# Optimization experiments

Hardware: AMD Instinct MI355X
Metric: run time of the kernel (lower is better)

The kernel has to match this reference:

```python
import jax, jax.numpy as jnp
import numpy as np

B, F, N, S, D = 128, 3, 64, 96, 64  # batch, features, nodes, steps, d_model
DIN = F + 1  # delta_t channel appended inside forward


def _layer_norm(x, g, b, eps=1e-5):
    mu = jnp.mean(x, -1, keepdims=True)
    var = jnp.mean((x - mu) ** 2, -1, keepdims=True)
    return (x - mu) * jax.lax.rsqrt(var + eps) * g + b


def _encoder_layer(x, inw, inb, ow, ob, w1, b1, w2, b2, g1, be1, g2, be2):
    # x: (B, N, D). Torch post-norm TransformerEncoderLayer, nhead=1, eval mode (no dropout).
    q, k, v = jnp.split(x @ inw.T + inb, 3, axis=-1)
    scores = jnp.einsum('bnd,bmd->bnm', q, k) / jnp.sqrt(jnp.asarray(D, x.dtype))
    a = jnp.einsum('bnm,bmd->bnd', jax.nn.softmax(scores, -1), v) @ ow.T + ob
    x = _layer_norm(x + a, g1, be1)
    ff = jax.nn.relu(x @ w1.T + b1) @ w2.T + b2
    return _layer_norm(x + ff, g2, be2)


def _diff_conv(x, adj, w, b):
    x1 = jnp.einsum('bcv,wv->bcw', x, adj)
    x2 = jnp.einsum('bcv,wv->bcw', x1, adj)
    z = jnp.concatenate([x, x1, x2], axis=1)  # (B, 3C, N)
    return jnp.einsum('bcn,oc->bon', z, w) + b[None, :, None]


def _forward(x, adj, h0, tp, uw, ub, cw, cb):
    times = x[:, 2, 0, :]  # (B, S) timestamps
    dt = jnp.concatenate([jnp.zeros((B, 1), x.dtype), times[:, 1:] - times[:, :-1]], axis=1)  # (B, S)
    xs = (jnp.transpose(x, (3, 0, 1, 2)), jnp.transpose(dt)[:, :, None])  # (S,B,F,N), (S,B,1)

    def step(h, inp):
        xt, d = inp  # (B,F,N), (B,1)
        xin = jnp.concatenate([xt, jnp.broadcast_to(d[:, :, None], (B, 1, N))], axis=1)  # (B,DIN,N)
        y = jnp.transpose(h, (0, 2, 1))  # (B, N, D): nodes are the attention sequence
        for i in range(2):
            y = _encoder_layer(y, *(a[i] for a in tp))
        eps = jnp.transpose(y, (0, 2, 1))  # (B, D, N)
        hd = jnp.sqrt(1.0 - d)[:, :, None] * h - jnp.sqrt(d)[:, :, None] * eps
        xg = jnp.concatenate([xin, hd], axis=1)  # (B, DIN+D, N)
        u = jax.nn.sigmoid(_diff_conv(xg, adj, uw, ub))
        c = jnp.tanh(_diff_conv(xg, adj, cw, cb))
        hn = u * hd + (1.0 - u) * c
        return hn, hn

    _, outs = jax.lax.scan(step, h0, xs)  # (S, B, D, N)
    return jnp.transpose(outs, (1, 3, 2, 0))  # (B, N, D, S) == stack().permute(1,3,2,0)


def setup_inputs() -> dict:
    key = jax.random.key(0)
    ks = jax.random.split(key, 12)
    s = 0.05
    x = jax.random.normal(ks[0], (B, F, N, S), jnp.float32)
    inc = jax.random.uniform(ks[1], (B, S), jnp.float32, 0.001, 0.01)
    x = x.at[:, 2, 0, :].set(jnp.cumsum(inc, axis=1))  # monotone times, delta_t in (0, 0.01)
    adj = jax.random.uniform(ks[2], (N, N), jnp.float32)
    adj = adj / jnp.sum(adj, axis=1, keepdims=True)
    h0 = jax.random.normal(ks[3], (B, D, N), jnp.float32)
    lengths = jax.random.randint(ks[4], (B,), 1, S, jnp.int32)  # unused by forward
    return {
        'x': x, 'adj': adj, 'lengths': lengths, 'h0': h0,
        't_inw': jax.random.normal(ks[5], (2, 3 * D, D), jnp.float32) * s,
        't_inb': jnp.zeros((2, 3 * D), jnp.float32),
        't_ow': jax.random.normal(ks[6], (2, D, D), jnp.float32) * s,
        't_ob': jnp.zeros((2, D), jnp.float32),
        't_w1': jax.random.normal(ks[7], (2, 64, D), jnp.float32) * s,
        't_b1': jnp.zeros((2, 64), jnp.float32),
        't_w2': jax.random.normal(ks[8], (2, D, 64), jnp.float32) * s,
        't_b2': jnp.zeros((2, D), jnp.float32),
        't_g1': jnp.ones((2, D), jnp.float32), 't_be1': jnp.zeros((2, D), jnp.float32),
        't_g2': jnp.ones((2, D), jnp.float32), 't_be2': jnp.zeros((2, D), jnp.float32),
        'uw': jax.random.normal(ks[9], (D, 3 * (DIN + D)), jnp.float32) * s,
        'ub': jnp.zeros((D,), jnp.float32),
        'cw': jax.random.normal(ks[10], (D, 3 * (DIN + D)), jnp.float32) * s,
        'cb': jnp.zeros((D,), jnp.float32),
    }


def reference(x, adj, lengths, h0, t_inw, t_inb, t_ow, t_ob, t_w1, t_b1, t_w2, t_b2,
              t_g1, t_be1, t_g2, t_be2, uw, ub, cw, cb):
    tp = (t_inw, t_inb, t_ow, t_ob, t_w1, t_b1, t_w2, t_b2, t_g1, t_be1, t_g2, t_be2)
    return _forward(x, adj, h0, tp, uw, ub, cw, cb)
```

## Files before the change

kernel.cpp:

```cpp
#include <hip/hip_runtime.h>
#include <math.h>

#define TPB 512

typedef __attribute__((ext_vector_type(8))) short bf16x8;
typedef __attribute__((ext_vector_type(4))) float f32x4;
typedef unsigned short u16;

#define MFMA(a, b, c) __builtin_amdgcn_mfma_f32_16x16x32_bf16(a, b, c, 0, 0, 0)

__device__ __forceinline__ u16 f2bf(float f) {
  union { float f; unsigned u; } v; v.f = f;
  unsigned u = v.u;
  return (u16)((u + 0x7fffu + ((u >> 16) & 1u)) >> 16);
}
__device__ __forceinline__ float bf2f(u16 h) {
  union { unsigned u; float f; } v; v.u = ((unsigned)h) << 16; return v.f;
}
__device__ __forceinline__ unsigned cvt2(float a0, float a1) {
  return (unsigned)f2bf(a0) | ((unsigned)f2bf(a1) << 16);
}
__device__ __forceinline__ void cvt4u(float a0, float a1, float a2, float a3, u16 o[4]) {
  o[0] = f2bf(a0); o[1] = f2bf(a1); o[2] = f2bf(a2); o[3] = f2bf(a3);
}

__device__ __forceinline__ bf16x8 fragL(const u16* B, int row0, int pitch, int kb, int lane) {
  return *(const bf16x8*)(B + (row0 + (lane & 15)) * pitch + kb + ((lane >> 4) << 3));
}
__device__ __forceinline__ bf16x8 fragG(const float* __restrict__ W, int row0, int stride,
                                        int kb, int lane) {
  const float* p = W + (size_t)(row0 + (lane & 15)) * stride + kb + ((lane >> 4) << 3);
  float4 a = *(const float4*)p, b = *(const float4*)(p + 4);
  bf16x8 r;
  r[0] = (short)f2bf(a.x); r[1] = (short)f2bf(a.y); r[2] = (short)f2bf(a.z); r[3] = (short)f2bf(a.w);
  r[4] = (short)f2bf(b.x); r[5] = (short)f2bf(b.y); r[6] = (short)f2bf(b.z); r[7] = (short)f2bf(b.w);
  return r;
}
template<int PREW>
__device__ __forceinline__ bf16x8 wfrag(const float* __restrict__ Wg,
                                        const u16* __restrict__ Wp,
                                        int m, int f, int kh, int lane) {
  if constexpr (PREW)
    return *(const bf16x8*)(Wp + (size_t)m * 4096 + f * 1024 + kh * 512 + lane * 8);
  else
    return fragG(Wg, f * 16, 64, kh * 32, lane);
}

__global__ __launch_bounds__(256)
void prep_kernel(const float* __restrict__ t_inw, const float* __restrict__ t_ow,
                 const float* __restrict__ t_w1, const float* __restrict__ t_w2,
                 const float* __restrict__ adj, const float* __restrict__ x,
                 u16* __restrict__ wp, u16* __restrict__ wpA2,
                 float* __restrict__ wsDT, u16* __restrict__ wsX) {
  int m = blockIdx.x;
  if (m == 12) {
    __shared__ float a2[4096];
    for (int e = threadIdx.x; e < 4096; e += 256) {
      int w = e >> 6, u = e & 63;
      float sum = 0.f;
      for (int v = 0; v < 64; ++v) sum += adj[w * 64 + v] * adj[v * 64 + u];
      a2[e] = sum;
    }
    __syncthreads();
    for (int t = threadIdx.x; t < 4096; t += 256) {
      int j = t & 7, ln = (t >> 3) & 63, kh = (t >> 9) & 1, f = t >> 10;
      int row = f * 16 + (ln & 15);
      int k = kh * 32 + ((ln >> 4) << 3) + j;
      wpA2[t] = f2bf(a2[row * 64 + k]);
    }
    return;
  }
  if (m >= 13) {
    int b = m - 13;
    const float* times = x + ((size_t)b * 3 + 2) * 64 * 96;
    for (int i = threadIdx.x; i < 96 * 256; i += 256) {
      int s = i >> 8, idx = i & 255, f = idx >> 6, n = idx & 63;
      float v;
      if (f < 3) v = x[(((size_t)b * 3 + f) * 64 + n) * 96 + s];
      else {
        float dt = s ? (times[s] - times[s - 1]) : 0.f;
        v = dt;
        if (n == 0) wsDT[b * 96 + s] = dt;
      }
      wsX[((size_t)b * 96 + s) * 256 + idx] = f2bf(v);
    }
    return;
  }
  int l = m / 6, r = m % 6;
  const float* W;
  if (r < 3)       W = t_inw + l * 12288 + r * 4096;
  else if (r == 3) W = t_ow + l * 4096;
  else if (r == 4) W = t_w1 + l * 4096;
  else             W = t_w2 + l * 4096;
  for (int t = threadIdx.x; t < 4096; t += 256) {
    int j = t & 7, ln = (t >> 3) & 63, kh = (t >> 9) & 1, f = t >> 10;
    int row = f * 16 + (ln & 15);
    int k = kh * 32 + ((ln >> 4) << 3) + j;
    wp[(size_t)m * 4096 + t] = f2bf(W[row * 64 + k]);
  }
}

__global__ __launch_bounds__(TPB, 2)
void gcrnn_fast(const float* __restrict__ adj,
                const float* __restrict__ h0,
                const float* __restrict__ t_inb, const float* __restrict__ t_ob,
                const float* __restrict__ t_b1,  const float* __restrict__ t_b2,
                const float* __restrict__ t_g1,  const float* __restrict__ t_be1,
                const float* __restrict__ t_g2,  const float* __restrict__ t_be2,
                const float* __restrict__ uw,    const float* __restrict__ ub,
                const float* __restrict__ cw,    const float* __restrict__ cb,
                const u16* __restrict__ wsW,  const u16* __restrict__ wsA2,
                const float* __restrict__ wsDT, const u16* __restrict__ wsX,
                float* __restrict__ wsOut)
{
  const int b = blockIdx.x;
  const int tid = threadIdx.x;
  const int wv = tid >> 6;
  const int lane = tid & 63;
  const int lx = lane & 15;
  const int gq = (lane >> 4) << 2;
  const int rs = wv & 3;
  const int of0 = (wv >> 2) * 2;
  const int fA = wv >> 2;

  __shared__ __align__(16) u16 adjB[64 * 72];
  __shared__ __align__(16) u16 Y0[64 * 72];
  __shared__ __align__(16) u16 Y1[64 * 72];
  __shared__ __align__(16) u16 Qb[64 * 72];
  __shared__ __align__(16) u16 Kb[64 * 72];
  __shared__ __align__(16) u16 VTb[64 * 72];
  __shared__ __align__(16) u16 Pb[64 * 72];
  __shared__ __align__(16) u16 xgB[80 * 72];
  __shared__ __align__(16) u16 zTB[64 * 232];
  __shared__ __align__(16) u16 uwcwB[2 * 4 * 7 * 512];

  float hreg[2][4];
  {
    const int nb = rs * 16 + gq;
#pragma unroll
    for (int ff = 0; ff < 2; ++ff) {
      int o = (of0 + ff) * 16 + lx;
      float4 hv = *(const float4*)(h0 + (size_t)b * 4096 + o * 64 + nb);
#pragma unroll
      for (int j = 0; j < 4; ++j) {
        hreg[ff][j] = (&hv.x)[j];
        Y0[(nb + j) * 72 + o] = f2bf(hreg[ff][j]);
      }
    }
  }
  for (int i = tid; i < 4096; i += TPB)
    adjB[(i >> 6) * 72 + (i & 63)] = f2bf(adj[i]);
  for (int i = tid; i < 2 * 4 * 7 * 512; i += TPB) {
    int t = i;
    int j = t & 7; t >>= 3;
    int ln = t & 63; t >>= 6;
    int kh = t % 7; t /= 7;
    int f = t & 3; int mat = t >> 2;
    int o = f * 16 + (ln & 15);
    int k = kh * 32 + ((ln >> 4) << 3) + j;
    const float* W = mat ? cw : uw;
    uwcwB[i] = (k < 204) ? f2bf(W[o * 204 + k]) : (u16)0;
  }
  for (int i = tid; i < 64 * 28; i += TPB)
    zTB[(i / 28) * 232 + 204 + (i % 28)] = 0;
  for (int i = tid; i < 12 * 72; i += TPB)
    xgB[68 * 72 + i] = 0;
  __syncthreads();

  const float buo = ub[of0 * 16 + lx], buo2 = ub[(of0 + 1) * 16 + lx];
  const float bco = cb[of0 * 16 + lx], bco2 = cb[(of0 + 1) * 16 + lx];
  float hdreg[2][4];

  for (int s = 0; s < 96; ++s) {
    float dcur = wsDT[b * 96 + s];
    float sq1 = sqrtf(1.f - dcur), sq2 = sqrtf(dcur);

    for (int l = 0; l < 2; ++l) {
      const int l6 = l * 6;
      const float* inb = t_inb + l * 192;
      const float* ob  = t_ob  + l * 64;
      const float* bb1 = t_b1  + l * 64;
      const float* bb2 = t_b2  + l * 64;
      const float* g1  = t_g1  + l * 64;
      const float* be1 = t_be1 + l * 64;
      const float* g2  = t_g2  + l * 64;
      const float* be2 = t_be2 + l * 64;

      bf16x8 fq[2][2], fk[2][2], fw1r[2][2], fvr[2];
#pragma unroll
      for (int fi = 0; fi < 2; ++fi)
#pragma unroll
        for (int kh = 0; kh < 2; ++kh) {
          fq[fi][kh]   = wfrag<1>(nullptr, wsW, l6 + 0, fA + fi * 2, kh, lane);
          fk[fi][kh]   = wfrag<1>(nullptr, wsW, l6 + 1, fA + fi * 2, kh, lane);
          fw1r[fi][kh] = wfrag<1>(nullptr, wsW, l6 + 4, fA + fi * 2, kh, lane);
        }
      if (wv >= 4) {
#pragma unroll
        for (int kh = 0; kh < 2; ++kh)
          fvr[kh] = wfrag<1>(nullptr, wsW, l6 + 2, rs, kh, lane);
      }

      {
        bf16x8 a0 = fragL(Y0, rs * 16, 72, 0, lane);
        bf16x8 a1 = fragL(Y0, rs * 16, 72, 32, lane);
#pragma unroll
        for (int fi = 0; fi < 2; ++fi) {
          int f = fA + fi * 2;
          int col = f * 16 + lx;
          {
            f32x4 acc = {0.f, 0.f, 0.f, 0.f};
            acc = MFMA(a0, fq[fi][0], acc);
            acc = MFMA(a1, fq[fi][1], acc);
            float bv = inb[col];
            u16 o4[4]; cvt4u(acc[0] + bv, acc[1] + bv, acc[2] + bv, acc[3] + bv, o4);
#pragma unroll
            for (int j = 0; j < 4; ++j)
              Qb[(rs * 16 + gq + j) * 72 + col] = o4[j];
          }
          {
            f32x4 acc = {0.f, 0.f, 0.f, 0.f};
            acc = MFMA(a0, fk[fi][0], acc);
            acc = MFMA(a1, fk[fi][1], acc);
            float bv = inb[64 + col];
            u16 o4[4]; cvt4u(acc[0] + bv, acc[1] + bv, acc[2] + bv, acc[3] + bv, o4);
#pragma unroll
            for (int j = 0; j < 4; ++j)
              Kb[(rs * 16 + gq + j) * 72 + col] = o4[j];
          }
        }
      }
      __syncthreads();

      if (wv < 4) {
        bf16x8 qa0 = fragL(Qb, rs * 16, 72, 0, lane);
        bf16x8 qa1 = fragL(Qb, rs * 16, 72, 32, lane);
        f32x4 sc[4];
#pragma unroll
        for (int f = 0; f < 4; ++f) {
          f32x4 acc = {0.f, 0.f, 0.f, 0.f};
          acc = MFMA(qa0, fragL(Kb, f * 16, 72, 0, lane), acc);
          acc = MFMA(qa1, fragL(Kb, f * 16, 72, 32, lane), acc);
#pragma unroll
          for (int j = 0; j < 4; ++j) acc[j] *= 0.125f;
          sc[f] = acc;
        }
#pragma unroll
        for (int j = 0; j < 4; ++j) {
          float m1 = fmaxf(fmaxf(sc[0][j], sc[1][j]), fmaxf(sc[2][j], sc[3][j]));
          m1 = fmaxf(m1, __shfl_xor(m1, 1));
          m1 = fmaxf(m1, __shfl_xor(m1, 2));
          m1 = fmaxf(m1, __shfl_xor(m1, 4));
          m1 = fmaxf(m1, __shfl_xor(m1, 8));
          float s1 = 0.f;
#pragma unroll
          for (int f = 0; f < 4; ++f) { float e = __expf(sc[f][j] - m1); sc[f][j] = e; s1 += e; }
          s1 += __shfl_xor(s1, 1); s1 += __shfl_xor(s1, 2);
          s1 += __shfl_xor(s1, 4); s1 += __shfl_xor(s1, 8);
          float inv = 1.f / s1;
          int row = rs * 16 + gq + j;
          u16 o4[4];
          cvt4u(sc[0][j] * inv, sc[1][j] * inv, sc[2][j] * inv, sc[3][j] * inv, o4);
#pragma unroll
          for (int f = 0; f < 4; ++f)
            Pb[row * 72 + f * 16 + lx] = o4[f];
        }
      } else {
#pragma unroll
        for (int f = 0; f < 4; ++f) {
          f32x4 acc = {0.f, 0.f, 0.f, 0.f};
          acc = MFMA(fvr[0], fragL(Y0, f * 16, 72, 0, lane), acc);
          acc = MFMA(fvr[1], fragL(Y0, f * 16, 72, 32, lane), acc);
          int dd0 = rs * 16 + gq;
          u16 o4[4];
          cvt4u(acc[0] + inb[128 + dd0], acc[1] + inb[128 + dd0 + 1],
                acc[2] + inb[128 + dd0 + 2], acc[3] + inb[128 + dd0 + 3], o4);
#pragma unroll
          for (int j = 0; j < 4; ++j)
            VTb[(dd0 + j) * 72 + f * 16 + lx] = o4[j];
        }
      }
      __syncthreads();

      bf16x8 fo[4][2];
      if (wv < 4) {
#pragma unroll
        for (int f = 0; f < 4; ++f)
#pragma unroll
          for (int kh = 0; kh < 2; ++kh)
            fo[f][kh] = wfrag<1>(nullptr, wsW, l6 + 3, f, kh, lane);
      }
      {
        bf16x8 pa0 = fragL(Pb, rs * 16, 72, 0, lane);
        bf16x8 pa1 = fragL(Pb, rs * 16, 72, 32, lane);
#pragma unroll
        for (int fi = 0; fi < 2; ++fi) {
          int f = fA + fi * 2;
          f32x4 acc = {0.f, 0.f, 0.f, 0.f};
          acc = MFMA(pa0, fragL(VTb, f * 16, 72, 0, lane), acc);
          acc = MFMA(pa1, fragL(VTb, f * 16, 72, 32, lane), acc);
          u16 o4[4]; cvt4u(acc[0], acc[1], acc[2], acc[3], o4);
#pragma unroll
          for (int j = 0; j < 4; ++j)
            Qb[(rs * 16 + gq + j) * 72 + f * 16 + lx] = o4[j];
        }
      }
      __syncthreads();

      if (wv < 4) {
        bf16x8 a0 = fragL(Qb, rs * 16, 72, 0, lane);
        bf16x8 a1 = fragL(Qb, rs * 16, 72, 32, lane);
        float t4[4][4];
#pragma unroll
        for (int f = 0; f < 4; ++f) {
          f32x4 acc = {0.f, 0.f, 0.f, 0.f};
          acc = MFMA(a0, fo[f][0], acc);
          acc = MFMA(a1, fo[f][1], acc);
          int col = f * 16 + lx;
          float bv = ob[col];
#pragma unroll
          for (int j = 0; j < 4; ++j) {
            int row = rs * 16 + gq + j;
            t4[f][j] = acc[j] + bv + bf2f(Y0[row * 72 + col]);
          }
        }
#pragma unroll
        for (int j = 0; j < 4; ++j) {
          float s1 = t4[0][j] + t4[1][j] + t4[2][j] + t4[3][j];
          float s2 = t4[0][j] * t4[0][j] + t4[1][j] * t4[1][j]
                   + t4[2][j] * t4[2][j] + t4[3][j] * t4[3][j];
          s1 += __shfl_xor(s1, 1); s2 += __shfl_xor(s2, 1);
          s1 += __shfl_xor(s1, 2); s2 += __shfl_xor(s2, 2);
          s1 += __shfl_xor(s1, 4); s2 += __shfl_xor(s2, 4);
          s1 += __shfl_xor(s1, 8); s2 += __shfl_xor(s2, 8);
          float mu = s1 * 0.015625f;
          float rstd = rsqrtf(s2 * 0.015625f - mu * mu + 1e-5f);
          int row = rs * 16 + gq + j;
          u16 o4[4];
          cvt4u((t4[0][j] - mu) * rstd * g1[0 * 16 + lx] + be1[0 * 16 + lx],
                (t4[1][j] - mu) * rstd * g1[1 * 16 + lx] + be1[1 * 16 + lx],
                (t4[2][j] - mu) * rstd * g1[2 * 16 + lx] + be1[2 * 16 + lx],
                (t4[3][j] - mu) * rstd * g1[3 * 16 + lx] + be1[3 * 16 + lx], o4);
#pragma unroll
          for (int f = 0; f < 4; ++f)
            Y1[row * 72 + f * 16 + lx] = o4[f];
        }
      }
      __syncthreads();

      bf16x8 fw2[4][2];
#pragma unroll
      for (int f = 0; f < 4; ++f)
#pragma unroll
        for (int kh = 0; kh < 2; ++kh)
          fw2[f][kh] = wfrag<1>(nullptr, wsW, l6 + 5, f, kh, lane);
      {
        bf16x8 a0 = fragL(Y1, rs * 16, 72, 0, lane);
        bf16x8 a1 = fragL(Y1, rs * 16, 72, 32, lane);
#pragma unroll
        for (int fi = 0; fi < 2; ++fi) {
          int f = fA + fi * 2;
          f32x4 acc = {0.f, 0.f, 0.f, 0.f};
          acc = MFMA(a0, fw1r[fi][0], acc);
          acc = MFMA(a1, fw1r[fi][1], acc);
          int col = f * 16 + lx;
          float bv = bb1[col];
          u16 o4[4];
          cvt4u(fmaxf(acc[0] + bv, 0.f), fmaxf(acc[1] + bv, 0.f),
                fmaxf(acc[2] + bv, 0.f), fmaxf(acc[3] + bv, 0.f), o4);
#pragma unroll
          for (int j = 0; j < 4; ++j)
            Kb[(rs * 16 + gq + j) * 72 + col] = o4[j];
        }
      }
      __syncthreads();

      if (l == 0) {
        if (wv < 4) {
          bf16x8 a0 = fragL(Kb, rs * 16, 72, 0, lane);
          bf16x8 a1 = fragL(Kb, rs * 16, 72, 32, lane);
          float t4[4][4];
#pragma unroll
          for (int f = 0; f < 4; ++f) {
            f32x4 acc = {0.f, 0.f, 0.f, 0.f};
            acc = MFMA(a0, fw2[f][0], acc);
            acc = MFMA(a1, fw2[f][1], acc);
            int col = f * 16 + lx;
            float bv = bb2[col];
#pragma unroll
            for (int j = 0; j < 4; ++j) {
              int row = rs * 16 + gq + j;
              t4[f][j] = acc[j] + bv + bf2f(Y1[row * 72 + col]);
            }
          }
#pragma unroll
          for (int j = 0; j < 4; ++j) {
            float s1 = t4[0][j] + t4[1][j] + t4[2][j] + t4[3][j];
            float s2 = t4[0][j] * t4[0][j] + t4[1][j] * t4[1][j]
                     + t4[2][j] * t4[2][j] + t4[3][j] * t4[3][j];
            s1 += __shfl_xor(s1, 1); s2 += __shfl_xor(s2, 1);
            s1 += __shfl_xor(s1, 2); s2 += __shfl_xor(s2, 2);
            s1 += __shfl_xor(s1, 4); s2 += __shfl_xor(s2, 4);
            s1 += __shfl_xor(s1, 8); s2 += __shfl_xor(s2, 8);
            float mu = s1 * 0.015625f;
            float rstd = rsqrtf(s2 * 0.015625f - mu * mu + 1e-5f);
            int row = rs * 16 + gq + j;
            u16 o4[4];
            cvt4u((t4[0][j] - mu) * rstd * g2[0 * 16 + lx] + be2[0 * 16 + lx],
                  (t4[1][j] - mu) * rstd * g2[1 * 16 + lx] + be2[1 * 16 + lx],
                  (t4[2][j] - mu) * rstd * g2[2 * 16 + lx] + be2[2 * 16 + lx],
                  (t4[3][j] - mu) * rstd * g2[3 * 16 + lx] + be2[3 * 16 + lx], o4);
#pragma unroll
            for (int f = 0; f < 4; ++f)
              Y0[row * 72 + f * 16 + lx] = o4[f];
          }
        }
      } else {
        bf16x8 a0 = fragL(Kb, rs * 16, 72, 0, lane);
        bf16x8 a1 = fragL(Kb, rs * 16, 72, 32, lane);
        float t4[4][4];
#pragma unroll
        for (int f = 0; f < 4; ++f) {
          f32x4 acc = {0.f, 0.f, 0.f, 0.f};
          acc = MFMA(a0, fw2[f][0], acc);
          acc = MFMA(a1, fw2[f][1], acc);
          int col = f * 16 + lx;
          float bv = bb2[col];
#pragma unroll
          for (int j = 0; j < 4; ++j) {
            int row = rs * 16 + gq + j;
            t4[f][j] = acc[j] + bv + bf2f(Y1[row * 72 + col]);
          }
        }
#pragma unroll
        for (int j = 0; j < 4; ++j) {
          float s1 = t4[0][j] + t4[1][j] + t4[2][j] + t4[3][j];
          float s2 = t4[0][j] * t4[0][j] + t4[1][j] * t4[1][j]
                   + t4[2][j] * t4[2][j] + t4[3][j] * t4[3][j];
          s1 += __shfl_xor(s1, 1); s2 += __shfl_xor(s2, 1);
          s1 += __shfl_xor(s1, 2); s2 += __shfl_xor(s2, 2);
          s1 += __shfl_xor(s1, 4); s2 += __shfl_xor(s2, 4);
          s1 += __shfl_xor(s1, 8); s2 += __shfl_xor(s2, 8);
          float mu = s1 * 0.015625f;
          float rstd = rsqrtf(s2 * 0.015625f - mu * mu + 1e-5f);
#pragma unroll
          for (int f = 0; f < 4; ++f) {
            int col = f * 16 + lx;
            t4[f][j] = (t4[f][j] - mu) * rstd * g2[col] + be2[col];
          }
        }
        {
          const u16* xr = wsX + ((size_t)b * 96 + s) * 256;
          for (int i = tid; i < 256; i += TPB) {
            u16 v = xr[i];
            int f = i >> 6, n = i & 63;
            xgB[f * 72 + n] = v;
            zTB[n * 232 + f] = v;
          }
        }
        const int nb = rs * 16 + gq;
#pragma unroll
        for (int f = 0; f < 4; ++f) {
          if ((f >> 1) == (wv >> 2)) {
            const int ff = f & 1;
            int o = f * 16 + lx;
            float hd0 = sq1 * hreg[ff][0] - sq2 * t4[f][0];
            float hd1 = sq1 * hreg[ff][1] - sq2 * t4[f][1];
            float hd2 = sq1 * hreg[ff][2] - sq2 * t4[f][2];
            float hd3 = sq1 * hreg[ff][3] - sq2 * t4[f][3];
            hdreg[ff][0] = hd0; hdreg[ff][1] = hd1;
            hdreg[ff][2] = hd2; hdreg[ff][3] = hd3;
            unsigned p0 = cvt2(hd0, hd1), p1 = cvt2(hd2, hd3);
            zTB[(nb + 0) * 232 + 4 + o] = (u16)p0;
            zTB[(nb + 1) * 232 + 4 + o] = (u16)(p0 >> 16);
            zTB[(nb + 2) * 232 + 4 + o] = (u16)p1;
            zTB[(nb + 3) * 232 + 4 + o] = (u16)(p1 >> 16);
            uint2 pk; pk.x = p0; pk.y = p1;
            *(uint2*)(xgB + (4 + o) * 72 + nb) = pk;
          }
        }
      }
      __syncthreads();
    }

    f32x4 aU0 = {0.f,0.f,0.f,0.f}, aU1 = {0.f,0.f,0.f,0.f};
    f32x4 aC0 = {0.f,0.f,0.f,0.f}, aC1 = {0.f,0.f,0.f,0.f};
    {
      bf16x8 g0 = *(const bf16x8*)(wsA2 + rs * 1024 + lane * 8);
      bf16x8 g1 = *(const bf16x8*)(wsA2 + rs * 1024 + 512 + lane * 8);
      bf16x8 aj0 = fragL(adjB, rs * 16, 72, 0, lane);
      bf16x8 aj1 = fragL(adjB, rs * 16, 72, 32, lane);

#define HT(A0, A1, CF, OFF) { \
      f32x4 acc = {0.f,0.f,0.f,0.f}; \
      acc = MFMA(A0, fragL(xgB, (CF) * 16, 72, 0, lane), acc); \
      acc = MFMA(A1, fragL(xgB, (CF) * 16, 72, 32, lane), acc); \
      int c = (CF) * 16 + lx; \
      if (c < 68) { u16 o4[4]; cvt4u(acc[0], acc[1], acc[2], acc[3], o4); \
        _Pragma("unroll") for (int j = 0; j < 4; ++j) \
          zTB[(rs * 16 + gq + j) * 232 + (OFF) + c] = o4[j]; } }

#define J01 { _Pragma("unroll") for (int kh = 0; kh < 2; ++kh) { \
      bf16x8 a = fragL(zTB, rs * 16, 232, kh * 32, lane); \
      { const u16* pu = uwcwB + (size_t)((of0 + 0) * 7 + kh) * 512 + lane * 8; \
        const u16* pc = uwcwB + (size_t)((4 + of0 + 0) * 7 + kh) * 512 + lane * 8; \
        aU0 = MFMA(a, *(const bf16x8*)pu, aU0); \
        aC0 = MFMA(a, *(const bf16x8*)pc, aC0); } \
      { const u16* pu = uwcwB + (size_t)((of0 + 1) * 7 + kh) * 512 + lane * 8; \
        const u16* pc = uwcwB + (size_t)((4 + of0 + 1) * 7 + kh) * 512 + lane * 8; \
        aU1 = MFMA(a, *(const bf16x8*)pu, aU1); \
        aC1 = MFMA(a, *(const bf16x8*)pc, aC1); } } }

      if (wv < 4) {
        HT(aj0, aj1, 0, 68); HT(aj0, aj1, 2, 68); HT(aj0, aj1, 4, 68);
        J01;
        HT(g0, g1, 1, 136); HT(g0, g1, 3, 136);
      } else {
        HT(aj0, aj1, 1, 68); HT(aj0, aj1, 3, 68);
        J01;
        HT(g0, g1, 0, 136); HT(g0, g1, 2, 136); HT(g0, g1, 4, 136);
      }
#undef HT
#undef J01
    }
    __syncthreads();

    {
#pragma unroll
      for (int kh = 2; kh < 7; ++kh) {
        bf16x8 a = fragL(zTB, rs * 16, 232, kh * 32, lane);
        {
          const u16* pu = uwcwB + (size_t)((of0 + 0) * 7 + kh) * 512 + lane * 8;
          const u16* pc = uwcwB + (size_t)((4 + of0 + 0) * 7 + kh) * 512 + lane * 8;
          aU0 = MFMA(a, *(const bf16x8*)pu, aU0);
          aC0 = MFMA(a, *(const bf16x8*)pc, aC0);
        }
        {
          const u16* pu = uwcwB + (size_t)((of0 + 1) * 7 + kh) * 512 + lane * 8;
          const u16* pc = uwcwB + (size_t)((4 + of0 + 1) * 7 + kh) * 512 + lane * 8;
          aU1 = MFMA(a, *(const bf16x8*)pu, aU1);
          aC1 = MFMA(a, *(const bf16x8*)pc, aC1);
        }
      }
      const int nb = rs * 16 + gq;
#pragma unroll
      for (int ff = 0; ff < 2; ++ff) {
        f32x4 aU = ff ? aU1 : aU0;
        f32x4 aC = ff ? aC1 : aC0;
        float bu_ = ff ? buo2 : buo;
        float bc_ = ff ? bco2 : bco;
        int o = (of0 + ff) * 16 + lx;
        float4 ov;
#pragma unroll
        for (int j = 0; j < 4; ++j) {
          float u = 1.f / (1.f + __expf(-(aU[j] + bu_)));
          float z = aC[j] + bc_;
          z = fminf(fmaxf(z, -15.f), 15.f);
          float e2 = __expf(2.f * z);
          float cval = (e2 - 1.f) / (e2 + 1.f);
          float hn = u * hdreg[ff][j] + (1.f - u) * cval;
          hreg[ff][j] = hn;
          (&ov.x)[j] = hn;
        }
        unsigned pk0 = cvt2(ov.x, ov.y), pk1 = cvt2(ov.z, ov.w);
        Y0[(nb + 0) * 72 + o] = (u16)pk0;
        Y0[(nb + 1) * 72 + o] = (u16)(pk0 >> 16);
        Y0[(nb + 2) * 72 + o] = (u16)pk1;
        Y0[(nb + 3) * 72 + o] = (u16)(pk1 >> 16);
        *(float4*)(wsOut + ((size_t)b * 96 + s) * 4096 + o * 64 + nb) = ov;
      }
    }
    __syncthreads();
  }
}

__global__ __launch_bounds__(TPB, 2)
void gcrnn_fb(const float* __restrict__ x, const float* __restrict__ adj,
              const float* __restrict__ h0,
              const float* __restrict__ t_inw, const float* __restrict__ t_inb,
              const float* __restrict__ t_ow,  const float* __restrict__ t_ob,
              const float* __restrict__ t_w1,  const float* __restrict__ t_b1,
              const float* __restrict__ t_w2,  const float* __restrict__ t_b2,
              const float* __restrict__ t_g1,  const float* __restrict__ t_be1,
              const float* __restrict__ t_g2,  const float* __restrict__ t_be2,
              const float* __restrict__ uw,    const float* __restrict__ ub,
              const float* __restrict__ cw,    const float* __restrict__ cb,
              float* __restrict__ out)
{
  const int b = blockIdx.x;
  const int tid = threadIdx.x;
  const int wv = tid >> 6;
  const int lane = tid & 63;
  const int lx = lane & 15;
  const int gq = (lane >> 4) << 2;
  const int rs = wv & 3;
  const int of0 = (wv >> 2) * 2;
  const int fA = wv >> 2;

  __shared__ __align__(16) u16 adjB[64 * 72];
  __shared__ __align__(16) u16 adj2B[64 * 72];
  __shared__ __align__(16) u16 ysB[64 * 72];
  __shared__ __align__(16) u16 pool[4 * 4608];
  __shared__ __align__(16) u16 zTB[64 * 232];
  __shared__ __align__(16) u16 uwcwB[2 * 4 * 7 * 512];

  u16* Qb  = pool;
  u16* Kb  = pool + 4608;
  u16* VTb = pool + 9216;
  u16* Pb  = pool + 13824;
  u16* xgB = pool;

  float hreg[2][4];
  {
    const int nb = rs * 16 + gq;
#pragma unroll
    for (int ff = 0; ff < 2; ++ff) {
      int o = (of0 + ff) * 16 + lx;
      float4 hv = *(const float4*)(h0 + (size_t)b * 4096 + o * 64 + nb);
#pragma unroll
      for (int j = 0; j < 4; ++j) {
        hreg[ff][j] = (&hv.x)[j];
        ysB[(nb + j) * 72 + o] = f2bf(hreg[ff][j]);
      }
    }
  }
  for (int i = tid; i < 4096; i += TPB)
    adjB[(i >> 6) * 72 + (i & 63)] = f2bf(adj[i]);
  for (int i = tid; i < 4096; i += TPB) {
    int w = i >> 6, u = i & 63;
    float sum = 0.f;
    for (int v = 0; v < 64; ++v) sum += adj[w * 64 + v] * adj[v * 64 + u];
    adj2B[w * 72 + u] = f2bf(sum);
  }
  for (int i = tid; i < 2 * 4 * 7 * 512; i += TPB) {
    int t = i;
    int j = t & 7; t >>= 3;
    int ln = t & 63; t >>= 6;
    int kh = t % 7; t /= 7;
    int f = t & 3; int mat = t >> 2;
    int o = f * 16 + (ln & 15);
    int k = kh * 32 + ((ln >> 4) << 3) + j;
    const float* W = mat ? cw : uw;
    uwcwB[i] = (k < 204) ? f2bf(W[o * 204 + k]) : (u16)0;
  }
  for (int i = tid; i < 64 * 28; i += TPB)
    zTB[(i / 28) * 232 + 204 + (i % 28)] = 0;
  __syncthreads();

  const float* times = x + ((size_t)b * 3 + 2) * 64 * 96;
  float hdreg[2][4];

  for (int s = 0; s < 96; ++s) {
    float dcur = (s == 0) ? 0.f : (times[s] - times[s - 1]);
    float sq1 = sqrtf(1.f - dcur), sq2 = sqrtf(dcur);

    for (int l = 0; l < 2; ++l) {
      const float* inw = t_inw + l * 12288;
      const float* inb = t_inb + l * 192;
      const float* ow  = t_ow  + l * 4096;
      const float* ob  = t_ob  + l * 64;
      const float* w1  = t_w1  + l * 4096;
      const float* bb1 = t_b1  + l * 64;
      const float* w2  = t_w2  + l * 4096;
      const float* bb2 = t_b2  + l * 64;
      const float* g1  = t_g1  + l * 64;
      const float* be1 = t_be1 + l * 64;
      const float* g2  = t_g2  + l * 64;
      const float* be2 = t_be2 + l * 64;

      {
        bf16x8 a0 = fragL(ysB, rs * 16, 72, 0, lane);
        bf16x8 a1 = fragL(ysB, rs * 16, 72, 32, lane);
#pragma unroll
        for (int fi = 0; fi < 2; ++fi) {
          int f = fA + fi * 2;
          int col = f * 16 + lx;
          {
            f32x4 acc = {0.f, 0.f, 0.f, 0.f};
            acc = MFMA(a0, fragG(inw, f * 16, 64, 0, lane), acc);
            acc = MFMA(a1, fragG(inw, f * 16, 64, 32, lane), acc);
            float bv = inb[col];
            u16 o4[4]; cvt4u(acc[0] + bv, acc[1] + bv, acc[2] + bv, acc[3] + bv, o4);
#pragma unroll
            for (int j = 0; j < 4; ++j)
              Qb[(rs * 16 + gq + j) * 72 + col] = o4[j];
          }
          {
            f32x4 acc = {0.f, 0.f, 0.f, 0.f};
            acc = MFMA(a0, fragG(inw + 4096, f * 16, 64, 0, lane), acc);
            acc = MFMA(a1, fragG(inw + 4096, f * 16, 64, 32, lane), acc);
            float bv = inb[64 + col];
            u16 o4[4]; cvt4u(acc[0] + bv, acc[1] + bv, acc[2] + bv, acc[3] + bv, o4);
#pragma unroll
            for (int j = 0; j < 4; ++j)
              Kb[(rs * 16 + gq + j) * 72 + col] = o4[j];
          }
        }
      }
      __syncthreads();

      if (wv < 4) {
        bf16x8 qa0 = fragL(Qb, rs * 16, 72, 0, lane);
        bf16x8 qa1 = fragL(Qb, rs * 16, 72, 32, lane);
        f32x4 sc[4];
#pragma unroll
        for (int f = 0; f < 4; ++f) {
          f32x4 acc = {0.f, 0.f, 0.f, 0.f};
          acc = MFMA(qa0, fragL(Kb, f * 16, 72, 0, lane), acc);
          acc = MFMA(qa1, fragL(Kb, f * 16, 72, 32, lane), acc);
#pragma unroll
          for (int j = 0; j < 4; ++j) acc[j] *= 0.125f;
          sc[f] = acc;
        }
#pragma unroll
        for (int j = 0; j < 4; ++j) {
          float m1 = fmaxf(fmaxf(sc[0][j], sc[1][j]), fmaxf(sc[2][j], sc[3][j]));
          m1 = fmaxf(m1, __shfl_xor(m1, 1));
          m1 = fmaxf(m1, __shfl_xor(m1, 2));
          m1 = fmaxf(m1, __shfl_xor(m1, 4));
          m1 = fmaxf(m1, __shfl_xor(m1, 8));
          float s1 = 0.f;
#pragma unroll
          for (int f = 0; f < 4; ++f) { float e = __expf(sc[f][j] - m1); sc[f][j] = e; s1 += e; }
          s1 += __shfl_xor(s1, 1); s1 += __shfl_xor(s1, 2);
          s1 += __shfl_xor(s1, 4); s1 += __shfl_xor(s1, 8);
          float inv = 1.f / s1;
          int row = rs * 16 + gq + j;
          u16 o4[4];
          cvt4u(sc[0][j] * inv, sc[1][j] * inv, sc[2][j] * inv, sc[3][j] * inv, o4);
#pragma unroll
          for (int f = 0; f < 4; ++f)
            Pb[row * 72 + f * 16 + lx] = o4[f];
        }
      } else {
        bf16x8 wa0 = fragG(inw + 8192, rs * 16, 64, 0, lane);
        bf16x8 wa1 = fragG(inw + 8192, rs * 16, 64, 32, lane);
#pragma unroll
        for (int f = 0; f < 4; ++f) {
          f32x4 acc = {0.f, 0.f, 0.f, 0.f};
          acc = MFMA(wa0, fragL(ysB, f * 16, 72, 0, lane), acc);
          acc = MFMA(wa1, fragL(ysB, f * 16, 72, 32, lane), acc);
          int dd0 = rs * 16 + gq;
          u16 o4[4];
          cvt4u(acc[0] + inb[128 + dd0], acc[1] + inb[128 + dd0 + 1],
                acc[2] + inb[128 + dd0 + 2], acc[3] + inb[128 + dd0 + 3], o4);
#pragma unroll
          for (int j = 0; j < 4; ++j)
            VTb[(dd0 + j) * 72 + f * 16 + lx] = o4[j];
        }
      }
      __syncthreads();

      {
        bf16x8 pa0 = fragL(Pb, rs * 16, 72, 0, lane);
        bf16x8 pa1 = fragL(Pb, rs * 16, 72, 32, lane);
#pragma unroll
        for (int fi = 0; fi < 2; ++fi) {
          int f = fA + fi * 2;
          f32x4 acc = {0.f, 0.f, 0.f, 0.f};
          acc = MFMA(pa0, fragL(VTb, f * 16, 72, 0, lane), acc);
          acc = MFMA(pa1, fragL(VTb, f * 16, 72, 32, lane), acc);
          u16 o4[4]; cvt4u(acc[0], acc[1], acc[2], acc[3], o4);
#pragma unroll
          for (int j = 0; j < 4; ++j)
            Qb[(rs * 16 + gq + j) * 72 + f * 16 + lx] = o4[j];
        }
      }
      __syncthreads();

      if (wv < 4) {
        bf16x8 a0 = fragL(Qb, rs * 16, 72, 0, lane);
        bf16x8 a1 = fragL(Qb, rs * 16, 72, 32, lane);
        float t4[4][4];
#pragma unroll
        for (int f = 0; f < 4; ++f) {
          f32x4 acc = {0.f, 0.f, 0.f, 0.f};
          acc = MFMA(a0, fragG(ow, f * 16, 64, 0, lane), acc);
          acc = MFMA(a1, fragG(ow, f * 16, 64, 32, lane), acc);
          int col = f * 16 + lx;
          float bv = ob[col];
#pragma unroll
          for (int j = 0; j < 4; ++j) {
            int row = rs * 16 + gq + j;
            t4[f][j] = acc[j] + bv + bf2f(ysB[row * 72 + col]);
          }
        }
#pragma unroll
        for (int j = 0; j < 4; ++j) {
          float s1 = t4[0][j] + t4[1][j] + t4[2][j] + t4[3][j];
          float s2 = t4[0][j] * t4[0][j] + t4[1][j] * t4[1][j]
                   + t4[2][j] * t4[2][j] + t4[3][j] * t4[3][j];
          s1 += __shfl_xor(s1, 1); s2 += __shfl_xor(s2, 1);
          s1 += __shfl_xor(s1, 2); s2 += __shfl_xor(s2, 2);
          s1 += __shfl_xor(s1, 4); s2 += __shfl_xor(s2, 4);
          s1 += __shfl_xor(s1, 8); s2 += __shfl_xor(s2, 8);
          float mu = s1 * 0.015625f;
          float rstd = rsqrtf(s2 * 0.015625f - mu * mu + 1e-5f);
          int row = rs * 16 + gq + j;
          u16 o4[4];
          cvt4u((t4[0][j] - mu) * rstd * g1[0 * 16 + lx] + be1[0 * 16 + lx],
                (t4[1][j] - mu) * rstd * g1[1 * 16 + lx] + be1[1 * 16 + lx],
                (t4[2][j] - mu) * rstd * g1[2 * 16 + lx] + be1[2 * 16 + lx],
                (t4[3][j] - mu) * rstd * g1[3 * 16 + lx] + be1[3 * 16 + lx], o4);
#pragma unroll
          for (int f = 0; f < 4; ++f)
            ysB[row * 72 + f * 16 + lx] = o4[f];
        }
      }
      __syncthreads();

      {
        bf16x8 a0 = fragL(ysB, rs * 16, 72, 0, lane);
        bf16x8 a1 = fragL(ysB, rs * 16, 72, 32, lane);
#pragma unroll
        for (int fi = 0; fi < 2; ++fi) {
          int f = fA + fi * 2;
          f32x4 acc = {0.f, 0.f, 0.f, 0.f};
          acc = MFMA(a0, fragG(w1, f * 16, 64, 0, lane), acc);
          acc = MFMA(a1, fragG(w1, f * 16, 64, 32, lane), acc);
          int col = f * 16 + lx;
          float bv = bb1[col];
          u16 o4[4];
          cvt4u(fmaxf(acc[0] + bv, 0.f), fmaxf(acc[1] + bv, 0.f),
                fmaxf(acc[2] + bv, 0.f), fmaxf(acc[3] + bv, 0.f), o4);
#pragma unroll
          for (int j = 0; j < 4; ++j)
            Kb[(rs * 16 + gq + j) * 72 + col] = o4[j];
        }
      }
      __syncthreads();

      if (wv < 4) {
        bf16x8 a0 = fragL(Kb, rs * 16, 72, 0, lane);
        bf16x8 a1 = fragL(Kb, rs * 16, 72, 32, lane);
        float t4[4][4];
#pragma unroll
        for (int f = 0; f < 4; ++f) {
          f32x4 acc = {0.f, 0.f, 0.f, 0.f};
          acc = MFMA(a0, fragG(w2, f * 16, 64, 0, lane), acc);
          acc = MFMA(a1, fragG(w2, f * 16, 64, 32, lane), acc);
          int col = f * 16 + lx;
          float bv = bb2[col];
#pragma unroll
          for (int j = 0; j < 4; ++j) {
            int row = rs * 16 + gq + j;
            t4[f][j] = acc[j] + bv + bf2f(ysB[row * 72 + col]);
          }
        }
#pragma unroll
        for (int j = 0; j < 4; ++j) {
          float s1 = t4[0][j] + t4[1][j] + t4[2][j] + t4[3][j];
          float s2 = t4[0][j] * t4[0][j] + t4[1][j] * t4[1][j]
                   + t4[2][j] * t4[2][j] + t4[3][j] * t4[3][j];
          s1 += __shfl_xor(s1, 1); s2 += __shfl_xor(s2, 1);
          s1 += __shfl_xor(s1, 2); s2 += __shfl_xor(s2, 2);
          s1 += __shfl_xor(s1, 4); s2 += __shfl_xor(s2, 4);
          s1 += __shfl_xor(s1, 8); s2 += __shfl_xor(s2, 8);
          float mu = s1 * 0.015625f;
          float rstd = rsqrtf(s2 * 0.015625f - mu * mu + 1e-5f);
          int row = rs * 16 + gq + j;
          u16 o4[4];
          cvt4u((t4[0][j] - mu) * rstd * g2[0 * 16 + lx] + be2[0 * 16 + lx],
                (t4[1][j] - mu) * rstd * g2[1 * 16 + lx] + be2[1 * 16 + lx],
                (t4[2][j] - mu) * rstd * g2[2 * 16 + lx] + be2[2 * 16 + lx],
                (t4[3][j] - mu) * rstd * g2[3 * 16 + lx] + be2[3 * 16 + lx], o4);
#pragma unroll
          for (int f = 0; f < 4; ++f)
            ysB[row * 72 + f * 16 + lx] = o4[f];
        }
      }
      __syncthreads();
    }

    {
      for (int i = tid; i < 256; i += TPB) {
        int f = i >> 6, n = i & 63;
        float v = (f < 3) ? x[(((size_t)b * 3 + f) * 64 + n) * 96 + s] : dcur;
        u16 v16 = f2bf(v);
        xgB[f * 72 + n] = v16;
        zTB[n * 232 + f] = v16;
      }
      const int nb = rs * 16 + gq;
#pragma unroll
      for (int ff = 0; ff < 2; ++ff) {
        int o = (of0 + ff) * 16 + lx;
        float hd0 = sq1 * hreg[ff][0] - sq2 * bf2f(ysB[(nb + 0) * 72 + o]);
        float hd1 = sq1 * hreg[ff][1] - sq2 * bf2f(ysB[(nb + 1) * 72 + o]);
        float hd2 = sq1 * hreg[ff][2] - sq2 * bf2f(ysB[(nb + 2) * 72 + o]);
        float hd3 = sq1 * hreg[ff][3] - sq2 * bf2f(ysB[(nb + 3) * 72 + o]);
        hdreg[ff][0] = hd0; hdreg[ff][1] = hd1; hdreg[ff][2] = hd2; hdreg[ff][3] = hd3;
        unsigned p0 = cvt2(hd0, hd1), p1 = cvt2(hd2, hd3);
        zTB[(nb + 0) * 232 + 4 + o] = (u16)p0;
        zTB[(nb + 1) * 232 + 4 + o] = (u16)(p0 >> 16);
        zTB[(nb + 2) * 232 + 4 + o] = (u16)p1;
        zTB[(nb + 3) * 232 + 4 + o] = (u16)(p1 >> 16);
        uint2 pk; pk.x = p0; pk.y = p1;
        *(uint2*)(xgB + (4 + o) * 72 + nb) = pk;
      }
    }
    __syncthreads();

    for (int t = wv; t < 40; t += 8) {
      int which = (t >= 20) ? 1 : 0;
      int tt = t - which * 20;
      int rw = tt & 3, cf = tt >> 2;
      const u16* A = which ? adj2B : adjB;
      f32x4 acc = {0.f, 0.f, 0.f, 0.f};
      acc = MFMA(fragL(A, rw * 16, 72, 0, lane), fragL(xgB, cf * 16, 72, 0, lane), acc);
      acc = MFMA(fragL(A, rw * 16, 72, 32, lane), fragL(xgB, cf * 16, 72, 32, lane), acc);
      int c = cf * 16 + lx;
      if (c < 68) {
        u16 o4[4]; cvt4u(acc[0], acc[1], acc[2], acc[3], o4);
#pragma unroll
        for (int j = 0; j < 4; ++j)
          zTB[(rw * 16 + gq + j) * 232 + 68 + which * 68 + c] = o4[j];
      }
    }
    __syncthreads();

    {
      f32x4 aU[2] = {{0.f,0.f,0.f,0.f},{0.f,0.f,0.f,0.f}};
      f32x4 aC[2] = {{0.f,0.f,0.f,0.f},{0.f,0.f,0.f,0.f}};
#pragma unroll
      for (int kh = 0; kh < 7; ++kh) {
        bf16x8 a = fragL(zTB, rs * 16, 232, kh * 32, lane);
#pragma unroll
        for (int ff = 0; ff < 2; ++ff) {
          int f = of0 + ff;
          const u16* pu = uwcwB + (size_t)((0 * 4 + f) * 7 + kh) * 512 + lane * 8;
          const u16* pc = uwcwB + (size_t)((1 * 4 + f) * 7 + kh) * 512 + lane * 8;
          aU[ff] = MFMA(a, *(const bf16x8*)pu, aU[ff]);
          aC[ff] = MFMA(a, *(const bf16x8*)pc, aC[ff]);
        }
      }
      const int nb = rs * 16 + gq;
#pragma unroll
      for (int ff = 0; ff < 2; ++ff) {
        int o = (of0 + ff) * 16 + lx;
        float bu_ = ub[o], bc_ = cb[o];
        float4 ov;
#pragma unroll
        for (int j = 0; j < 4; ++j) {
          float u = 1.f / (1.f + __expf(-(aU[ff][j] + bu_)));
          float z = aC[ff][j] + bc_;
          z = fminf(fmaxf(z, -15.f), 15.f);
          float e2 = __expf(2.f * z);
          float cval = (e2 - 1.f) / (e2 + 1.f);
          float hn = u * hdreg[ff][j] + (1.f - u) * cval;
          hreg[ff][j] = hn;
          (&ov.x)[j] = hn;
        }
        unsigned pk0 = cvt2(ov.x, ov.y), pk1 = cvt2(ov.z, ov.w);
        ysB[(nb + 0) * 72 + o] = (u16)pk0;
        ysB[(nb + 1) * 72 + o] = (u16)(pk0 >> 16);
        ysB[(nb + 2) * 72 + o] = (u16)pk1;
        ysB[(nb + 3) * 72 + o] = (u16)(pk1 >> 16);
#pragma unroll
        for (int j = 0; j < 4; ++j)
          out[((size_t)(b * 64 + (nb + j)) * 64 + o) * 96 + s] = (&ov.x)[j];
      }
    }
    __syncthreads();
  }
}

__global__ __launch_bounds__(256)
void transp_kernel(const float* __restrict__ ws, float* __restrict__ out) {
  int blk = blockIdx.x;
  int b = blk >> 6, o = blk & 63;
  __shared__ float t[96 * 68];
  for (int i = threadIdx.x; i < 96 * 64; i += 256) {
    int ss = i >> 6, n = i & 63;
    t[ss * 68 + n] = ws[((size_t)b * 96 + ss) * 4096 + o * 64 + n];
  }
  __syncthreads();
  for (int i = threadIdx.x; i < 64 * 96; i += 256) {
    int n = i / 96, ss = i - n * 96;
    out[((size_t)(b * 64 + n) * 64 + o) * 96 + ss] = t[ss * 68 + n];
  }
}

extern "C" void kernel_launch(void* const* d_in, const int* in_sizes, int n_in,
                              void* d_out, int out_size, void* d_ws, size_t ws_size,
                              hipStream_t stream)
{
  (void)in_sizes; (void)n_in; (void)out_size;
  const float* x     = (const float*)d_in[0];
  const float* adj   = (const float*)d_in[1];
  const float* h0    = (const float*)d_in[3];
  const float* t_inw = (const float*)d_in[4];
  const float* t_inb = (const float*)d_in[5];
  const float* t_ow  = (const float*)d_in[6];
  const float* t_ob  = (const float*)d_in[7];
  const float* t_w1  = (const float*)d_in[8];
  const float* t_b1  = (const float*)d_in[9];
  const float* t_w2  = (const float*)d_in[10];
  const float* t_b2  = (const float*)d_in[11];
  const float* t_g1  = (const float*)d_in[12];
  const float* t_be1 = (const float*)d_in[13];
  const float* t_g2  = (const float*)d_in[14];
  const float* t_be2 = (const float*)d_in[15];
  const float* uw    = (const float*)d_in[16];
  const float* ub    = (const float*)d_in[17];
  const float* cw    = (const float*)d_in[18];
  const float* cb    = (const float*)d_in[19];
  float* out = (float*)d_out;

  const size_t offA2    = 98304;
  const size_t offDT    = 106496;
  const size_t offX     = 155648;
  const size_t offStage = 6447104;
  const size_t stageBytes = (size_t)128 * 96 * 4096 * 4;

  if (ws_size >= offStage + stageBytes) {
    u16*   wsW   = (u16*)d_ws;
    u16*   wsA2  = (u16*)((char*)d_ws + offA2);
    float* wsDT  = (float*)((char*)d_ws + offDT);
    u16*   wsX   = (u16*)((char*)d_ws + offX);
    float* wsOut = (float*)((char*)d_ws + offStage);

    hipLaunchKernelGGL(prep_kernel, dim3(141), dim3(256), 0, stream,
                       t_inw, t_ow, t_w1, t_w2, adj, x, wsW, wsA2, wsDT, wsX);
    hipLaunchKernelGGL(gcrnn_fast, dim3(128), dim3(TPB), 0, stream,
                       adj, h0, t_inb, t_ob, t_b1, t_b2, t_g1, t_be1, t_g2, t_be2,
                       uw, ub, cw, cb, wsW, wsA2, wsDT, wsX, wsOut);
    hipLaunchKernelGGL(transp_kernel, dim3(128 * 64), dim3(256), 0, stream, wsOut, out);
  } else {
    hipLaunchKernelGGL(gcrnn_fb, dim3(128), dim3(TPB), 0, stream,
                       x, adj, h0, t_inw, t_inb, t_ow, t_ob, t_w1, t_b1,
                       t_w2, t_b2, t_g1, t_be1, t_g2, t_be2, uw, ub, cw, cb, out);
  }
}
```

Baseline: 1.498 ms.

## Give each wave full row-strips to drop intra-layer and diffusion-conv barriers

```diff
diff --git a/kernel.cpp b/kernel.cpp
--- a/kernel.cpp
+++ b/kernel.cpp
@@ -186,14 +186,13 @@
       const float* g2  = t_g2  + l * 64;
       const float* be2 = t_be2 + l * 64;
 
-      bf16x8 fq[2][2], fk[2][2], fw1r[2][2], fvr[2];
+      bf16x8 fq[2][2], fk[2][2], fvr[2];
 #pragma unroll
       for (int fi = 0; fi < 2; ++fi)
 #pragma unroll
         for (int kh = 0; kh < 2; ++kh) {
-          fq[fi][kh]   = wfrag<1>(nullptr, wsW, l6 + 0, fA + fi * 2, kh, lane);
-          fk[fi][kh]   = wfrag<1>(nullptr, wsW, l6 + 1, fA + fi * 2, kh, lane);
-          fw1r[fi][kh] = wfrag<1>(nullptr, wsW, l6 + 4, fA + fi * 2, kh, lane);
+          fq[fi][kh] = wfrag<1>(nullptr, wsW, l6 + 0, fA + fi * 2, kh, lane);
+          fk[fi][kh] = wfrag<1>(nullptr, wsW, l6 + 1, fA + fi * 2, kh, lane);
         }
       if (wv >= 4) {
 #pragma unroll
@@ -282,101 +281,93 @@
       }
       __syncthreads();
 
-      bf16x8 fo[4][2];
       if (wv < 4) {
+        bf16x8 fo[4][2], fw1[4][2];
 #pragma unroll
         for (int f = 0; f < 4; ++f)
 #pragma unroll
-          for (int kh = 0; kh < 2; ++kh)
-            fo[f][kh] = wfrag<1>(nullptr, wsW, l6 + 3, f, kh, lane);
-      }
-      {
-        bf16x8 pa0 = fragL(Pb, rs * 16, 72, 0, lane);
-        bf16x8 pa1 = fragL(Pb, rs * 16, 72, 32, lane);
-#pragma unroll
-        for (int fi = 0; fi < 2; ++fi) {
-          int f = fA + fi * 2;
-          f32x4 acc = {0.f, 0.f, 0.f, 0.f};
-          acc = MFMA(pa0, fragL(VTb, f * 16, 72, 0, lane), acc);
-          acc = MFMA(pa1, fragL(VTb, f * 16, 72, 32, lane), acc);
-          u16 o4[4]; cvt4u(acc[0], acc[1], acc[2], acc[3], o4);
-#pragma unroll
-          for (int j = 0; j < 4; ++j)
-            Qb[(rs * 16 + gq + j) * 72 + f * 16 + lx] = o4[j];
-        }
-      }
-      __syncthreads();
-
-      if (wv < 4) {
-        bf16x8 a0 = fragL(Qb, rs * 16, 72, 0, lane);
-        bf16x8 a1 = fragL(Qb, rs * 16, 72, 32, lane);
-        float t4[4][4];
-#pragma unroll
-        for (int f = 0; f < 4; ++f) {
-          f32x4 acc = {0.f, 0.f, 0.f, 0.f};
-          acc = MFMA(a0, fo[f][0], acc);
-          acc = MFMA(a1, fo[f][1], acc);
-          int col = f * 16 + lx;
-          float bv = ob[col];
+          for (int kh = 0; kh < 2; ++kh) {
+            fo[f][kh]  = wfrag<1>(nullptr, wsW, l6 + 3, f, kh, lane);
+            fw1[f][kh] = wfrag<1>(nullptr, wsW, l6 + 4, f, kh, lane);
+          }
+        {
+          bf16x8 pa0 = fragL(Pb, rs * 16, 72, 0, lane);
+          bf16x8 pa1 = fragL(Pb, rs * 16, 72, 32, lane);
+#pragma unroll
+          for (int f = 0; f < 4; ++f) {
+            f32x4 acc = {0.f, 0.f, 0.f, 0.f};
+            acc = MFMA(pa0, fragL(VTb, f * 16, 72, 0, lane), acc);
+            acc = MFMA(pa1, fragL(VTb, f * 16, 72, 32, lane), acc);
+            u16 o4[4]; cvt4u(acc[0], acc[1], acc[2], acc[3], o4);
+#pragma unroll
+            for (int j = 0; j < 4; ++j)
+              Qb[(rs * 16 + gq + j) * 72 + f * 16 + lx] = o4[j];
+          }
+        }
+        {
+          bf16x8 a0 = fragL(Qb, rs * 16, 72, 0, lane);
+          bf16x8 a1 = fragL(Qb, rs * 16, 72, 32, lane);
+          float t4[4][4];
+#pragma unroll
+          for (int f = 0; f < 4; ++f) {
+            f32x4 acc = {0.f, 0.f, 0.f, 0.f};
+            acc = MFMA(a0, fo[f][0], acc);
+            acc = MFMA(a1, fo[f][1], acc);
+            int col = f * 16 + lx;
+            float bv = ob[col];
+#pragma unroll
+            for (int j = 0; j < 4; ++j) {
+              int row = rs * 16 + gq + j;
+              t4[f][j] = acc[j] + bv + bf2f(Y0[row * 72 + col]);
+            }
+          }
 #pragma unroll
           for (int j = 0; j < 4; ++j) {
+            float s1 = t4[0][j] + t4[1][j] + t4[2][j] + t4[3][j];
+            float s2 = t4[0][j] * t4[0][j] + t4[1][j] * t4[1][j]
+                     + t4[2][j] * t4[2][j] + t4[3][j] * t4[3][j];
+            s1 += __shfl_xor(s1, 1); s2 += __shfl_xor(s2, 1);
+            s1 += __shfl_xor(s1, 2); s2 += __shfl_xor(s2, 2);
+            s1 += __shfl_xor(s1, 4); s2 += __shfl_xor(s2, 4);
+            s1 += __shfl_xor(s1, 8); s2 += __shfl_xor(s2, 8);
+            float mu = s1 * 0.015625f;
+            float rstd = rsqrtf(s2 * 0.015625f - mu * mu + 1e-5f);
             int row = rs * 16 + gq + j;
-            t4[f][j] = acc[j] + bv + bf2f(Y0[row * 72 + col]);
-          }
-        }
-#pragma unroll
-        for (int j = 0; j < 4; ++j) {
-          float s1 = t4[0][j] + t4[1][j] + t4[2][j] + t4[3][j];
-          float s2 = t4[0][j] * t4[0][j] + t4[1][j] * t4[1][j]
-                   + t4[2][j] * t4[2][j] + t4[3][j] * t4[3][j];
-          s1 += __shfl_xor(s1, 1); s2 += __shfl_xor(s2, 1);
-          s1 += __shfl_xor(s1, 2); s2 += __shfl_xor(s2, 2);
-          s1 += __shfl_xor(s1, 4); s2 += __shfl_xor(s2, 4);
-          s1 += __shfl_xor(s1, 8); s2 += __shfl_xor(s2, 8);
-          float mu = s1 * 0.015625f;
-          float rstd = rsqrtf(s2 * 0.015625f - mu * mu + 1e-5f);
-          int row = rs * 16 + gq + j;
-          u16 o4[4];
-          cvt4u((t4[0][j] - mu) * rstd * g1[0 * 16 + lx] + be1[0 * 16 + lx],
-                (t4[1][j] - mu) * rstd * g1[1 * 16 + lx] + be1[1 * 16 + lx],
-                (t4[2][j] - mu) * rstd * g1[2 * 16 + lx] + be1[2 * 16 + lx],
-                (t4[3][j] - mu) * rstd * g1[3 * 16 + lx] + be1[3 * 16 + lx], o4);
+            u16 o4[4];
+            cvt4u((t4[0][j] - mu) * rstd * g1[0 * 16 + lx] + be1[0 * 16 + lx],
+                  (t4[1][j] - mu) * rstd * g1[1 * 16 + lx] + be1[1 * 16 + lx],
+                  (t4[2][j] - mu) * rstd * g1[2 * 16 + lx] + be1[2 * 16 + lx],
+                  (t4[3][j] - mu) * rstd * g1[3 * 16 + lx] + be1[3 * 16 + lx], o4);
+#pragma unroll
+            for (int f = 0; f < 4; ++f)
+              Y1[row * 72 + f * 16 + lx] = o4[f];
+          }
+        }
+        {
+          bf16x8 a0 = fragL(Y1, rs * 16, 72, 0, lane);
+          bf16x8 a1 = fragL(Y1, rs * 16, 72, 32, lane);
+#pragma unroll
+          for (int f = 0; f < 4; ++f) {
+            f32x4 acc = {0.f, 0.f, 0.f, 0.f};
+            acc = MFMA(a0, fw1[f][0], acc);
+            acc = MFMA(a1, fw1[f][1], acc);
+            int col = f * 16 + lx;
+            float bv = bb1[col];
+            u16 o4[4];
+            cvt4u(fmaxf(acc[0] + bv, 0.f), fmaxf(acc[1] + bv, 0.f),
+                  fmaxf(acc[2] + bv, 0.f), fmaxf(acc[3] + bv, 0.f), o4);
+#pragma unroll
+            for (int j = 0; j < 4; ++j)
+              Kb[(rs * 16 + gq + j) * 72 + col] = o4[j];
+          }
+        }
+        if (l == 0) {
+          bf16x8 fw2[4][2];
 #pragma unroll
           for (int f = 0; f < 4; ++f)
-            Y1[row * 72 + f * 16 + lx] = o4[f];
-        }
-      }
-      __syncthreads();
-
-      bf16x8 fw2[4][2];
-#pragma unroll
-      for (int f = 0; f < 4; ++f)
-#pragma unroll
-        for (int kh = 0; kh < 2; ++kh)
-          fw2[f][kh] = wfrag<1>(nullptr, wsW, l6 + 5, f, kh, lane);
-      {
-        bf16x8 a0 = fragL(Y1, rs * 16, 72, 0, lane);
-        bf16x8 a1 = fragL(Y1, rs * 16, 72, 32, lane);
-#pragma unroll
-        for (int fi = 0; fi < 2; ++fi) {
-          int f = fA + fi * 2;
-          f32x4 acc = {0.f, 0.f, 0.f, 0.f};
-          acc = MFMA(a0, fw1r[fi][0], acc);
-          acc = MFMA(a1, fw1r[fi][1], acc);
-          int col = f * 16 + lx;
-          float bv = bb1[col];
-          u16 o4[4];
-          cvt4u(fmaxf(acc[0] + bv, 0.f), fmaxf(acc[1] + bv, 0.f),
-                fmaxf(acc[2] + bv, 0.f), fmaxf(acc[3] + bv, 0.f), o4);
-#pragma unroll
-          for (int j = 0; j < 4; ++j)
-            Kb[(rs * 16 + gq + j) * 72 + col] = o4[j];
-        }
-      }
-      __syncthreads();
-
-      if (l == 0) {
-        if (wv < 4) {
+#pragma unroll
+            for (int kh = 0; kh < 2; ++kh)
+              fw2[f][kh] = wfrag<1>(nullptr, wsW, l6 + 5, f, kh, lane);
           bf16x8 a0 = fragL(Kb, rs * 16, 72, 0, lane);
           bf16x8 a1 = fragL(Kb, rs * 16, 72, 32, lane);
           float t4[4][4];
@@ -415,7 +406,16 @@
               Y0[row * 72 + f * 16 + lx] = o4[f];
           }
         }
-      } else {
+      }
+      __syncthreads();
+
+      if (l == 1) {
+        bf16x8 fw2[4][2];
+#pragma unroll
+        for (int f = 0; f < 4; ++f)
+#pragma unroll
+          for (int kh = 0; kh < 2; ++kh)
+            fw2[f][kh] = wfrag<1>(nullptr, wsW, l6 + 5, f, kh, lane);
         bf16x8 a0 = fragL(Kb, rs * 16, 72, 0, lane);
         bf16x8 a1 = fragL(Kb, rs * 16, 72, 32, lane);
         float t4[4][4];
@@ -479,13 +479,13 @@
             *(uint2*)(xgB + (4 + o) * 72 + nb) = pk;
           }
         }
-      }
-      __syncthreads();
+        __syncthreads();
+      }
     }
 
-    f32x4 aU0 = {0.f,0.f,0.f,0.f}, aU1 = {0.f,0.f,0.f,0.f};
-    f32x4 aC0 = {0.f,0.f,0.f,0.f}, aC1 = {0.f,0.f,0.f,0.f};
     {
+      f32x4 aU0 = {0.f,0.f,0.f,0.f}, aU1 = {0.f,0.f,0.f,0.f};
+      f32x4 aC0 = {0.f,0.f,0.f,0.f}, aC1 = {0.f,0.f,0.f,0.f};
       bf16x8 g0 = *(const bf16x8*)(wsA2 + rs * 1024 + lane * 8);
       bf16x8 g1 = *(const bf16x8*)(wsA2 + rs * 1024 + 512 + lane * 8);
       bf16x8 aj0 = fragL(adjB, rs * 16, 72, 0, lane);
@@ -500,32 +500,28 @@
         _Pragma("unroll") for (int j = 0; j < 4; ++j) \
           zTB[(rs * 16 + gq + j) * 232 + (OFF) + c] = o4[j]; } }
 
-#define J01 { _Pragma("unroll") for (int kh = 0; kh < 2; ++kh) { \
-      bf16x8 a = fragL(zTB, rs * 16, 232, kh * 32, lane); \
-      { const u16* pu = uwcwB + (size_t)((of0 + 0) * 7 + kh) * 512 + lane * 8; \
-        const u16* pc = uwcwB + (size_t)((4 + of0 + 0) * 7 + kh) * 512 + lane * 8; \
-        aU0 = MFMA(a, *(const bf16x8*)pu, aU0); \
-        aC0 = MFMA(a, *(const bf16x8*)pc, aC0); } \
-      { const u16* pu = uwcwB + (size_t)((of0 + 1) * 7 + kh) * 512 + lane * 8; \
-        const u16* pc = uwcwB + (size_t)((4 + of0 + 1) * 7 + kh) * 512 + lane * 8; \
-        aU1 = MFMA(a, *(const bf16x8*)pu, aU1); \
-        aC1 = MFMA(a, *(const bf16x8*)pc, aC1); } } }
-
-      if (wv < 4) {
-        HT(aj0, aj1, 0, 68); HT(aj0, aj1, 2, 68); HT(aj0, aj1, 4, 68);
-        J01;
-        HT(g0, g1, 1, 136); HT(g0, g1, 3, 136);
-      } else {
-        HT(aj0, aj1, 1, 68); HT(aj0, aj1, 3, 68);
-        J01;
-        HT(g0, g1, 0, 136); HT(g0, g1, 2, 136); HT(g0, g1, 4, 136);
-      }
+      HT(aj0, aj1, 0, 68); HT(aj0, aj1, 1, 68); HT(aj0, aj1, 2, 68);
+      HT(aj0, aj1, 3, 68); HT(aj0, aj1, 4, 68);
+#pragma unroll
+      for (int kh = 0; kh < 2; ++kh) {
+        bf16x8 a = fragL(zTB, rs * 16, 232, kh * 32, lane);
+        {
+          const u16* pu = uwcwB + (size_t)((of0 + 0) * 7 + kh) * 512 + lane * 8;
+          const u16* pc = uwcwB + (size_t)((4 + of0 + 0) * 7 + kh) * 512 + lane * 8;
+          aU0 = MFMA(a, *(const bf16x8*)pu, aU0);
+          aC0 = MFMA(a, *(const bf16x8*)pc, aC0);
+        }
+        {
+          const u16* pu = uwcwB + (size_t)((of0 + 1) * 7 + kh) * 512 + lane * 8;
+          const u16* pc = uwcwB + (size_t)((4 + of0 + 1) * 7 + kh) * 512 + lane * 8;
+          aU1 = MFMA(a, *(const bf16x8*)pu, aU1);
+          aC1 = MFMA(a, *(const bf16x8*)pc, aC1);
+        }
+      }
+      HT(g0, g1, 0, 136); HT(g0, g1, 1, 136); HT(g0, g1, 2, 136);
+      HT(g0, g1, 3, 136); HT(g0, g1, 4, 136);
 #undef HT
-#undef J01
-    }
-    __syncthreads();
-
-    {
+
 #pragma unroll
       for (int kh = 2; kh < 7; ++kh) {
         bf16x8 a = fragL(zTB, rs * 16, 232, kh * 32, lane);
```

Result: faster. 1.447 ms (-3.4%).
